# Optimization experiments

Hardware: AMD Instinct MI355X
Metric: run time of the kernel (lower is better)

The kernel has to match this reference:

```python
import jax, jax.numpy as jnp
import numpy as np
from jax.scipy.linalg import solve_triangular

B, K, N = 64, 24, 934  # batch, SMPL joints (key_size), sparse mesh points (A_size)
LAMBDA_FACTOR = 1.0


def _rodrigues(rvec):
    # rvec: [..., 3] axis-angle -> [..., 3, 3] rotation matrix (SMPL rodrigues)
    theta = jnp.maximum(jnp.linalg.norm(rvec, axis=-1, keepdims=True), 1e-8)
    a = rvec / theta
    c = jnp.cos(theta)[..., None]
    s = jnp.sin(theta)[..., None]
    ax, ay, az = a[..., 0], a[..., 1], a[..., 2]
    zero = jnp.zeros_like(ax)
    skew = jnp.stack([
        jnp.stack([zero, -az, ay], -1),
        jnp.stack([az, zero, -ax], -1),
        jnp.stack([-ay, ax, zero], -1)], -2)
    aaT = a[..., :, None] * a[..., None, :]
    eye = jnp.eye(3, dtype=rvec.dtype)
    return c * eye + s * skew + (1.0 - c) * aaT


def setup_inputs() -> dict:
    key = jax.random.key(0)
    ks = jax.random.split(key, 8)
    return {
        "uv_curr": jax.random.uniform(ks[0], (B, N, 2), jnp.float32),
        "xm_": jax.random.normal(ks[1], (B, K, N, 3), jnp.float32),
        "b_s_": jax.random.normal(ks[2], (B, K, N, 3, 10), jnp.float32) * 0.1,
        "blend_curr": jax.random.uniform(ks[3], (N, K), jnp.float32),
        "W": jax.random.uniform(ks[4], (B, N), jnp.float32) * 0.95 + 0.05,
        "m00": jnp.ones((B,), jnp.float32),
        "m11": jnp.ones((B,), jnp.float32),
        "m02": jax.random.uniform(ks[5], (B,), jnp.float32),
        "m12": jax.random.uniform(ks[6], (B,), jnp.float32),
        "pred_beta": jax.random.normal(ks[7], (B, 10), jnp.float32),
        "valid_R_list_stack": jnp.broadcast_to(jnp.eye(4, dtype=jnp.float32), (B, K, 4, 4)),
    }


def reference(uv_curr, xm_, b_s_, blend_curr, W, m00, m11, m02, m12, pred_beta, valid_R_list_stack):
    Bn, Kn, Nn = xm_.shape[0], xm_.shape[1], xm_.shape[2]
    lam = jnp.exp(jnp.log(jnp.float32(1.0 / 3.0)) * jnp.float32(LAMBDA_FACTOR))  # k0*exp(log(k0/3)*lf)

    bT = blend_curr.T[None]                      # [1,K,N]
    f0 = m00[:, None, None]                       # [B,1,1]
    f1 = m11[:, None, None]
    dxu = (m02[:, None] - uv_curr[..., 0])[:, None]  # [B,1,N]
    dyv = (m12[:, None] - uv_curr[..., 1])[:, None]

    x1 = dxu * xm_[..., 1]
    x2 = f0 * xm_[..., 2] - dxu * xm_[..., 0]
    x3 = -f0 * xm_[..., 1]
    x8 = jnp.broadcast_to(bT * f0, (Bn, Kn, Nn))
    x9 = jnp.zeros((Bn, Kn, Nn), xm_.dtype)
    x10 = jnp.broadcast_to(bT * dxu, (Bn, Kn, Nn))
    y1 = -f1 * xm_[..., 2] + dyv * xm_[..., 1]
    y2 = -dyv * xm_[..., 0]
    y3 = f1 * xm_[..., 0]
    y8 = x9
    y9 = jnp.broadcast_to(bT * f1, (Bn, Kn, Nn))
    y10 = jnp.broadcast_to(bT * dyv, (Bn, Kn, Nn))

    # shape-beta blocks: [B,K,N,10]
    x4a = f0[..., None] * b_s_[:, :, :, 0] + dxu[..., None] * b_s_[:, :, :, 2]
    y4a = f1[..., None] * b_s_[:, :, :, 1] + dyv[..., None] * b_s_[:, :, :, 2]

    b1 = -f0 * xm_[..., 0] - dxu * xm_[..., 2]
    b2 = -f1 * xm_[..., 1] - dyv * xm_[..., 2]

    # [B,K,N,6] -> [B,N,K*6]
    A1 = jnp.stack([x1, x2, x3, x8, x9, x10], -1).transpose(0, 2, 1, 3).reshape(Bn, Nn, Kn * 6)
    A2 = jnp.stack([y1, y2, y3, y8, y9, y10], -1).transpose(0, 2, 1, 3).reshape(Bn, Nn, Kn * 6)
    Wn = W[..., None]
    A_top = jnp.concatenate([Wn * A1, Wn * A2], 1)            # [B,2N,6K]
    A_sh = jnp.concatenate([Wn * x4a.sum(1), Wn * y4a.sum(1)], 1)  # [B,2N,10]
    b_top = jnp.concatenate([W * b1.sum(1), W * b2.sum(1)], 1)     # [B,2N]

    rows = 2 * Nn + 10 + 3 * Kn + 3
    cols = 6 * Kn + 10
    A = jnp.zeros((Bn, rows, cols), jnp.float32)
    A = A.at[:, :2 * Nn, :6 * Kn].set(A_top)
    A = A.at[:, :2 * Nn, 6 * Kn:].set(A_sh)
    ridx = jnp.arange(10)
    A = A.at[:, rows - 10 + ridx, cols - 10 + ridx].set(lam)  # beta regularizer
    Bv = jnp.zeros((Bn, rows), jnp.float32)
    Bv = Bv.at[:, :2 * Nn].set(b_top)
    Bv = Bv.at[:, rows - 10:].set(lam * pred_beta)

    # least squares via reduced QR (same as torch train path / lstsq solution)
    q, r = jnp.linalg.qr(A)                       # q:[B,rows,cols], r:[B,cols,cols]
    rhs = jnp.einsum('bmn,bm->bn', q, Bv)
    sol = solve_triangular(r, rhs[..., None], lower=False)[..., 0]  # [B,6K+10]

    rt6 = sol[:, :6 * Kn].reshape(Bn, Kn, 6)
    r_pred = _rodrigues(rt6[..., :3])             # [B,K,3,3]
    t_pred = rt6[..., 3:]                         # [B,K,3]
    bottom = jnp.broadcast_to(jnp.array([0.0, 0.0, 0.0, 1.0], jnp.float32), (Bn, Kn, 1, 4))
    rt_pred = jnp.concatenate([
        jnp.concatenate([r_pred, jnp.zeros((Bn, Kn, 3, 1), jnp.float32)], -1),
        bottom], -2)                               # [B,K,4,4]
    r_curr = rt_pred @ valid_R_list_stack
    beta = sol[:, -10:]
    return (r_curr, t_pred, beta, r_pred)
```

## Files before the change

kernel.cpp:

```cpp
#include <hip/hip_runtime.h>
#include <hip/hip_bf16.h>

#define Bn 64
#define Kn 24
#define Nn 934
#define NBLK 4
#define GCH 234
#define NPTS 16
#define RNDS 15
#define GPK 12090
#define PB 11
#define NPAN 14
#define ST 512
#define STR 168
#define GT 512
#define MAXT 9

#define G_BYTES ((size_t)Bn * GPK * 8)

typedef __attribute__((ext_vector_type(4))) double f64x4;

__device__ __forceinline__ int rb(int i) { return (i * (i + 1)) >> 1; }

__global__ __launch_bounds__(1024) void k_pre(
    const float* __restrict__ uv, const float* __restrict__ xm,
    const float* __restrict__ bs, const float* __restrict__ Wp,
    const float* __restrict__ m00, const float* __restrict__ m11,
    const float* __restrict__ m02, const float* __restrict__ m12,
    float* __restrict__ pre)
{
    __shared__ float smL[32][30];
    __shared__ float xsL[32][3];
    const int tid = threadIdx.x;
    const int b = blockIdx.y;
    const int n0 = blockIdx.x * 32;
    const float f0 = m00[b], f1 = m11[b], cx = m02[b], cy = m12[b];

    if (tid < 960) {
        const int ni = tid / 30, c = tid - ni * 30;
        const int nc = min(n0 + ni, Nn - 1);
        float acc = 0.0f;
        const float* bp = bs + ((size_t)(b * Kn) * Nn + nc) * 30 + c;
        #pragma unroll
        for (int k = 0; k < Kn; ++k) acc += bp[(size_t)k * Nn * 30];
        smL[ni][c] = acc;
    } else {
        const int v = tid - 960;
        #pragma unroll
        for (int rep = 0; rep < 2; ++rep) {
            const int w = v + rep * 64;
            if (w < 96) {
                const int ni = w / 3, c = w - ni * 3;
                const int nc = min(n0 + ni, Nn - 1);
                float acc = 0.0f;
                const float* xp = xm + ((size_t)(b * Kn) * Nn + nc) * 3 + c;
                #pragma unroll
                for (int k = 0; k < Kn; ++k) acc += xp[(size_t)k * Nn * 3];
                xsL[ni][c] = acc;
            }
        }
    }
    __syncthreads();

    if (tid < 704) {
        const int ni = tid / 22, e = tid - ni * 22;
        const int n = n0 + ni;
        if (n < Nn) {
            const float u = uv[((size_t)b * Nn + n) * 2 + 0];
            const float v = uv[((size_t)b * Nn + n) * 2 + 1];
            const float w = Wp[(size_t)b * Nn + n];
            const float dxu = cx - u, dyv = cy - v;
            float val;
            if (e < 10)       val = w * (f0 * smL[ni][e] + dxu * smL[ni][20 + e]);
            else if (e < 20)  val = w * (f1 * smL[ni][e] + dyv * smL[ni][e + 10]);
            else if (e == 20) val = w * (-f0 * xsL[ni][0] - dxu * xsL[ni][2]);
            else              val = w * (-f1 * xsL[ni][1] - dyv * xsL[ni][2]);
            pre[((size_t)b * Nn + n) * 22 + e] = val;
        }
    }
}

__global__ __launch_bounds__(GT, 1) void k_gram(
    const float* __restrict__ uv, const float* __restrict__ xm,
    const float* __restrict__ blend, const float* __restrict__ Wp,
    const float* __restrict__ m00, const float* __restrict__ m11,
    const float* __restrict__ m02, const float* __restrict__ m12,
    const float* __restrict__ pre, double* __restrict__ Gpk)
{
    __shared__ float rowsF[2][2 * NPTS][STR];
    const int tid = threadIdx.x;
    const int b = blockIdx.y;
    const int n0 = blockIdx.x * GCH;
    const int nEnd = min(n0 + GCH, Nn);
    const float f0 = m00[b], f1 = m11[b], cx = m02[b], cy = m12[b];

    const int pt = (tid >> 4) & 15, s = tid & 15;
    const int wave = tid >> 6, lane = tid & 63;

    const f64x4 zz = {0.0, 0.0, 0.0, 0.0};
    const f64x4 pr = __builtin_amdgcn_mfma_f64_16x16x4f64((double)lane, 1.0, zz, 0, 0, 0);
    const f64x4 pc = __builtin_amdgcn_mfma_f64_16x16x4f64(1.0, (double)lane, zz, 0, 0, 0);
    const int v0 = (int)pr[0];
    const bool ac0 = (v0 >= 96) && (v0 <= 156) && (((v0 - 96) & 3) == 0);
    const int arow = ac0 ? (lane & 15) : (lane >> 2);
    const int ak   = ac0 ? (lane >> 4) : (lane & 3);
    const int w0 = (int)pc[0];
    const bool bc0 = (w0 >= 96) && (w0 <= 156) && (((w0 - 96) & 3) == 0);
    const int bcol = bc0 ? (lane & 15) : (lane >> 2);
    const int bk   = bc0 ? (lane >> 4) : (lane & 3);
    int orow[4], ocol[4];
    #pragma unroll
    for (int r2 = 0; r2 < 4; ++r2) {
        const int vr = (int)pr[r2];
        orow[r2] = ac0 ? ((vr - 96) >> 2) : ((vr - 6) >> 4);
        const int wr = (int)pc[r2];
        ocol[r2] = bc0 ? ((wr - 96) >> 2) : ((wr - 6) >> 4);
    }

    const int t0 = (wave < 4) ? wave * 5 : 20 + (wave - 4) * 9;
    const int cnt = (wave < 4) ? 5 : 9;
    int Ia[MAXT], Ja[MAXT];
    {
        int Iv = 0, Jv = t0;
        while (Jv > Iv) { Jv -= (Iv + 1); ++Iv; }
        #pragma unroll
        for (int t = 0; t < MAXT; ++t) {
            Ia[t] = Iv; Ja[t] = Jv;
            ++Jv;
            if (Jv > Iv) { Jv = 0; ++Iv; }
        }
    }

    f64x4 acc[MAXT];
    #pragma unroll
    for (int t = 0; t < MAXT; ++t) acc[t] = (f64x4){0.0, 0.0, 0.0, 0.0};

    float pf[11];
    const bool isBd = tid < 256;

    auto PF = [&](int rnd) {
        if (!isBd) return;
        const int nc = min(n0 + rnd * NPTS + pt, Nn - 1);
        if (s < 12) {
            const int k0 = 2 * s;
            const float* xa = xm + ((size_t)(b * Kn + k0) * Nn + nc) * 3;
            const float* xb = xm + ((size_t)(b * Kn + k0 + 1) * Nn + nc) * 3;
            pf[0] = xa[0]; pf[1] = xa[1]; pf[2] = xa[2];
            pf[3] = xb[0]; pf[4] = xb[1]; pf[5] = xb[2];
            pf[6] = blend[nc * Kn + k0];
            pf[7] = blend[nc * Kn + k0 + 1];
            pf[8] = uv[((size_t)b * Nn + nc) * 2 + 0];
            pf[9] = uv[((size_t)b * Nn + nc) * 2 + 1];
            pf[10] = Wp[(size_t)b * Nn + nc];
        } else if (s < 15) {
            const int e0 = (s - 12) * 8;
            const float* pp = pre + ((size_t)b * Nn + nc) * 22;
            #pragma unroll
            for (int j = 0; j < 8; ++j) pf[j] = (e0 + j < 22) ? pp[e0 + j] : 0.0f;
        }
    };
    auto WR = [&](int rnd, int bufi) {
        if (!isBd) return;
        const int n = n0 + rnd * NPTS + pt;
        float* rx = &rowsF[bufi][2 * pt][0];
        float* ry = &rowsF[bufi][2 * pt + 1][0];
        if (s < 12) {
            #pragma unroll
            for (int jj = 0; jj < 2; ++jj) {
                float vx[6], vy[6];
                if (n < nEnd) {
                    const float x0 = pf[jj * 3 + 0], x1 = pf[jj * 3 + 1], x2 = pf[jj * 3 + 2];
                    const float dxu = cx - pf[8], dyv = cy - pf[9], w = pf[10];
                    const float wbl = w * pf[6 + jj];
                    vx[0] = w * dxu * x1; vx[1] = w * (f0 * x2 - dxu * x0); vx[2] = -w * f0 * x1;
                    vx[3] = wbl * f0;     vx[4] = 0.0f;                     vx[5] = wbl * dxu;
                    vy[0] = w * (dyv * x1 - f1 * x2); vy[1] = -w * dyv * x0; vy[2] = w * f1 * x0;
                    vy[3] = 0.0f;         vy[4] = wbl * f1;                 vy[5] = wbl * dyv;
                } else {
                    #pragma unroll
                    for (int e = 0; e < 6; ++e) { vx[e] = 0.0f; vy[e] = 0.0f; }
                }
                const int cb = 6 * (2 * s + jj);
                #pragma unroll
                for (int e = 0; e < 6; ++e) {
                    rx[cb + e] = vx[e];
                    ry[cb + e] = vy[e];
                }
            }
        } else if (s < 15) {
            const int e0 = (s - 12) * 8;
            #pragma unroll
            for (int j = 0; j < 8; ++j) {
                const int e = e0 + j;
                if (e < 22) {
                    const float val = (n < nEnd) ? pf[j] : 0.0f;
                    if (e < 10)       rx[144 + e] = val;
                    else if (e < 20)  ry[144 + (e - 10)] = val;
                    else if (e == 20) rx[154] = val;
                    else              ry[154] = val;
                }
            }
        }
    };

    for (int idx = tid; idx < 320; idx += GT) {
        const int bufi = idx / 160, rem = idx % 160;
        rowsF[bufi][rem / 5][155 + rem % 5] = 0.0f;
    }

    PF(0);
    WR(0, 0);
    PF(1);
    __syncthreads();

    for (int r = 0; r < RNDS; ++r) {
        const int cur = r & 1;
        if (r < RNDS - 1) {
            WR(r + 1, cur ^ 1);
            if (r + 2 < RNDS) PF(r + 2);
        }
        #pragma unroll
        for (int ksl = 0; ksl < 8; ++ksl) {
            const float* rowA = &rowsF[cur][4 * ksl + ak][0];
            const float* rowB = &rowsF[cur][4 * ksl + bk][0];
            #pragma unroll
            for (int t = 0; t < MAXT; ++t) {
                if (t < cnt && t0 + t < 55) {
                    const double av = (double)rowA[16 * Ia[t] + arow];
                    const double bv = (double)rowB[16 * Ja[t] + bcol];
                    acc[t] = __builtin_amdgcn_mfma_f64_16x16x4f64(av, bv, acc[t], 0, 0, 0);
                }
            }
        }
        __syncthreads();
    }

    double* Gb = Gpk + (size_t)b * GPK;
    #pragma unroll
    for (int t = 0; t < MAXT; ++t) {
        if (t < cnt && t0 + t < 55) {
            #pragma unroll
            for (int rr = 0; rr < 4; ++rr) {
                const int gi = 16 * Ia[t] + orow[rr];
                const int gj = 16 * Ja[t] + ocol[rr];
                if (gi < 155 && gj < 155 && gj <= gi)
                    unsafeAtomicAdd(&Gb[rb(gi) + gj], acc[t][rr]);
            }
        }
    }
}

__global__ __launch_bounds__(ST, 2) void k_solve(
    const float* __restrict__ pbeta, const float* __restrict__ vR,
    const double* __restrict__ Gpk, float* __restrict__ out)
{
    __shared__ double tri[12090];
    __shared__ double fd[NPAN][66];
    __shared__ double Pp[144][PB];
    __shared__ double Qq[144][PB];
    __shared__ double cv[160];
    __shared__ double xv[160];
    __shared__ double dinv[160];
    const int tid = threadIdx.x;
    const int b = blockIdx.x;
    const double lam2 = 1.0 / 9.0;
    const double* Gb = Gpk + (size_t)b * GPK;

    for (int idx = tid; idx < GPK; idx += ST) tri[idx] = Gb[idx];
    __syncthreads();
    if (tid < 10) {
        const int d = 144 + tid;
        tri[rb(d) + d] += lam2;
        tri[rb(154) + 144 + tid] += lam2 * (double)pbeta[b * 10 + tid];
    }
    __syncthreads();

    for (int p = 0; p < NPAN; ++p) {
        const int c0 = p * PB, r0 = c0 + PB;
        const int m2 = 155 - r0;

        double dblk[66], dl[PB];
        #pragma unroll
        for (int r = 0; r < PB; ++r) {
            const int baser = rb(c0 + r) + c0;
            #pragma unroll
            for (int c = 0; c <= r; ++c) dblk[r * (r + 1) / 2 + c] = tri[baser + c];
        }
        #pragma unroll
        for (int j = 0; j < PB; ++j) {
            const double invd = 1.0 / dblk[j * (j + 1) / 2 + j];
            dl[j] = invd;
            #pragma unroll
            for (int r = j + 1; r < PB; ++r) {
                const double mr = dblk[r * (r + 1) / 2 + j] * invd;
                #pragma unroll
                for (int c = j + 1; c <= r; ++c)
                    dblk[r * (r + 1) / 2 + c] -= mr * dblk[c * (c + 1) / 2 + j];
            }
        }
        if (tid == 0) {
            #pragma unroll
            for (int e = 0; e < 66; ++e) fd[p][e] = dblk[e];
            #pragma unroll
            for (int j = 0; j < PB; ++j) dinv[c0 + j] = dl[j];
        }

        for (int i = r0 + tid; i < 155; i += ST) {
            const int ip = i - r0;
            const int base = rb(i) + c0;
            double a[PB], bbv[PB];
            #pragma unroll
            for (int k = 0; k < PB; ++k) a[k] = tri[base + k];
            #pragma unroll
            for (int t = 0; t < PB; ++t) {
                const double bt = a[t] * dl[t];
                bbv[t] = bt;
                #pragma unroll
                for (int k = t + 1; k < PB; ++k)
                    a[k] -= bt * dblk[k * (k + 1) / 2 + t];
            }
            #pragma unroll
            for (int k = 0; k < PB; ++k) {
                tri[base + k] = a[k]; Pp[ip][k] = bbv[k]; Qq[ip][k] = a[k];
            }
        }
        __syncthreads();

        {
            const int th2 = (m2 + 1) >> 1;
            const int ttot = (th2 * (th2 + 1)) >> 1;
            for (int e = tid; e < ttot; e += ST) {
                int tr = (int)((sqrtf(8.0f * (float)e + 1.0f) - 1.0f) * 0.5f);
                while ((tr + 1) * (tr + 2) / 2 <= e) ++tr;
                while (tr * (tr + 1) / 2 > e) --tr;
                const int tc = e - ((tr * (tr + 1)) >> 1);
                const int rg0 = 2 * tr, cg0 = 2 * tc;
                const bool r1ok = (rg0 + 1) < m2;
                const bool c1ok = (cg0 + 1) < m2;
                double pa0[PB], pa1[PB], qb0[PB], qb1[PB];
                #pragma unroll
                for (int k = 0; k < PB; ++k) {
                    pa0[k] = Pp[rg0][k];
                    pa1[k] = r1ok ? Pp[rg0 + 1][k] : 0.0;
                    qb0[k] = Qq[cg0][k];
                    qb1[k] = c1ok ? Qq[cg0 + 1][k] : 0.0;
                }
                double s00 = 0.0, s01 = 0.0, s10 = 0.0, s11 = 0.0;
                #pragma unroll
                for (int k = 0; k < PB; ++k) {
                    s00 += pa0[k] * qb0[k];
                    s01 += pa0[k] * qb1[k];
                    s10 += pa1[k] * qb0[k];
                    s11 += pa1[k] * qb1[k];
                }
                tri[rb(r0 + rg0) + r0 + cg0] -= s00;
                if (c1ok && (cg0 + 1) <= rg0)
                    tri[rb(r0 + rg0) + r0 + cg0 + 1] -= s01;
                if (r1ok)
                    tri[rb(r0 + rg0 + 1) + r0 + cg0] -= s10;
                if (r1ok && c1ok)
                    tri[rb(r0 + rg0 + 1) + r0 + cg0 + 1] -= s11;
            }
        }
        __syncthreads();
    }

    for (int j = tid; j < 154; j += ST) xv[j] = tri[rb(154) + j] * dinv[j];
    __syncthreads();

    for (int p = NPAN - 1; p >= 0; --p) {
        const int c0 = p * PB;
        double x[PB], dl[PB];
        #pragma unroll
        for (int r = 0; r < PB; ++r) { dl[r] = dinv[c0 + r]; x[r] = xv[c0 + r]; }
        #pragma unroll
        for (int j = PB - 1; j >= 1; --j) {
            #pragma unroll
            for (int i2 = 0; i2 < j; ++i2)
                x[i2] -= dl[i2] * fd[p][j * (j + 1) / 2 + i2] * x[j];
        }
        if (tid == 0) {
            #pragma unroll
            for (int r = 0; r < PB; ++r) cv[c0 + r] = x[r];
        }
        for (int i = tid; i < c0; i += ST) {
            double sum = 0.0;
            #pragma unroll
            for (int jj = 0; jj < PB; ++jj) sum += tri[rb(c0 + jj) + i] * x[jj];
            xv[i] -= dinv[i] * sum;
        }
        __syncthreads();
    }

    if (tid < Kn) {
        const int k = tid;
        const double rxv = cv[6 * k + 0], ryv = cv[6 * k + 1], rzv = cv[6 * k + 2];
        const double t0 = cv[6 * k + 3], t1 = cv[6 * k + 4], t2 = cv[6 * k + 5];
        const double nrm = sqrt(rxv * rxv + ryv * ryv + rzv * rzv);
        const double th = fmax(nrm, 1e-8);
        const double ax = rxv / th, ay = ryv / th, az = rzv / th;
        const double c = cos(th), sn = sin(th), mc = 1.0 - c;
        double R[3][3];
        R[0][0] = c + mc * ax * ax;        R[0][1] = -sn * az + mc * ax * ay; R[0][2] =  sn * ay + mc * ax * az;
        R[1][0] =  sn * az + mc * ay * ax; R[1][1] = c + mc * ay * ay;        R[1][2] = -sn * ax + mc * ay * az;
        R[2][0] = -sn * ay + mc * az * ax; R[2][1] =  sn * ax + mc * az * ay; R[2][2] = c + mc * az * az;

        const float* VRp = vR + ((size_t)(b * Kn + k)) * 16;
        float* oc = out + ((size_t)(b * Kn + k)) * 16;
        #pragma unroll
        for (int r = 0; r < 3; ++r)
            #pragma unroll
            for (int cc = 0; cc < 4; ++cc) {
                const double val = R[r][0] * (double)VRp[0 * 4 + cc]
                                 + R[r][1] * (double)VRp[1 * 4 + cc]
                                 + R[r][2] * (double)VRp[2 * 4 + cc];
                oc[r * 4 + cc] = (float)val;
            }
        #pragma unroll
        for (int cc = 0; cc < 4; ++cc) oc[12 + cc] = VRp[12 + cc];

        float* ot = out + 24576 + ((size_t)(b * Kn + k)) * 3;
        ot[0] = (float)t0; ot[1] = (float)t1; ot[2] = (float)t2;

        float* orp = out + 29824 + ((size_t)(b * Kn + k)) * 9;
        #pragma unroll
        for (int r = 0; r < 3; ++r)
            #pragma unroll
            for (int cc = 0; cc < 3; ++cc)
                orp[r * 3 + cc] = (float)R[r][cc];
    }
    if (tid >= 32 && tid < 42) {
        out[29184 + b * 10 + (tid - 32)] = (float)cv[144 + (tid - 32)];
    }
}

extern "C" void kernel_launch(void* const* d_in, const int* in_sizes, int n_in,
                              void* d_out, int out_size, void* d_ws, size_t ws_size,
                              hipStream_t stream) {
    const float* uv    = (const float*)d_in[0];
    const float* xm    = (const float*)d_in[1];
    const float* bs    = (const float*)d_in[2];
    const float* blend = (const float*)d_in[3];
    const float* Wp    = (const float*)d_in[4];
    const float* m00   = (const float*)d_in[5];
    const float* m11   = (const float*)d_in[6];
    const float* m02   = (const float*)d_in[7];
    const float* m12   = (const float*)d_in[8];
    const float* pbeta = (const float*)d_in[9];
    const float* vRp   = (const float*)d_in[10];
    float* out = (float*)d_out;
    double* Gpk = (double*)d_ws;
    float* pre = (float*)((char*)d_ws + G_BYTES);

    hipMemsetAsync(d_ws, 0, G_BYTES, stream);

    dim3 gP((Nn + 31) / 32, Bn);
    k_pre<<<gP, 1024, 0, stream>>>(uv, xm, bs, Wp, m00, m11, m02, m12, pre);

    dim3 gG(NBLK, Bn);
    k_gram<<<gG, GT, 0, stream>>>(uv, xm, blend, Wp, m00, m11, m02, m12, pre, Gpk);

    k_solve<<<Bn, ST, 0, stream>>>(pbeta, vRp, Gpk, out);
}
```

Baseline: 229.2 us.

## Transpose Gram shared tile to column-major for vectorized MFMA operand loads

The shared-memory staging buffer for the Gram-matrix rows is transposed so that each column holds the 32 row samples contiguously (padded stride 36). Each lane can then fetch its eight k-values with two float4 LDS reads instead of eight scalar reads, and the MFMA chain per tile runs back-to-back. Each lane now sums its k-values in a different order, but the result is still the same A^T A product. The write side now scatters scalars across columns, which may cause bank conflicts there.

```diff
diff --git a/kernel.cpp b/kernel.cpp
--- a/kernel.cpp
+++ b/kernel.cpp
@@ -12,7 +12,7 @@
 #define PB 11
 #define NPAN 14
 #define ST 512
-#define STR 168
+#define CSTR 36
 #define GT 512
 #define MAXT 9
 
@@ -87,7 +87,7 @@
     const float* __restrict__ m02, const float* __restrict__ m12,
     const float* __restrict__ pre, double* __restrict__ Gpk)
 {
-    __shared__ float rowsF[2][2 * NPTS][STR];
+    __shared__ float rowsT[2][160][CSTR];
     const int tid = threadIdx.x;
     const int b = blockIdx.y;
     const int n0 = blockIdx.x * GCH;
@@ -162,8 +162,7 @@
     auto WR = [&](int rnd, int bufi) {
         if (!isBd) return;
         const int n = n0 + rnd * NPTS + pt;
-        float* rx = &rowsF[bufi][2 * pt][0];
-        float* ry = &rowsF[bufi][2 * pt + 1][0];
+        const int rx = 2 * pt, ry = 2 * pt + 1;
         if (s < 12) {
             #pragma unroll
             for (int jj = 0; jj < 2; ++jj) {
@@ -183,8 +182,8 @@
                 const int cb = 6 * (2 * s + jj);
                 #pragma unroll
                 for (int e = 0; e < 6; ++e) {
-                    rx[cb + e] = vx[e];
-                    ry[cb + e] = vy[e];
+                    rowsT[bufi][cb + e][rx] = vx[e];
+                    rowsT[bufi][cb + e][ry] = vy[e];
                 }
             }
         } else if (s < 15) {
@@ -194,10 +193,10 @@
                 const int e = e0 + j;
                 if (e < 22) {
                     const float val = (n < nEnd) ? pf[j] : 0.0f;
-                    if (e < 10)       rx[144 + e] = val;
-                    else if (e < 20)  ry[144 + (e - 10)] = val;
-                    else if (e == 20) rx[154] = val;
-                    else              ry[154] = val;
+                    if (e < 10)       rowsT[bufi][144 + e][rx] = val;
+                    else if (e < 20)  rowsT[bufi][144 + (e - 10)][ry] = val;
+                    else if (e == 20) rowsT[bufi][154][rx] = val;
+                    else              rowsT[bufi][154][ry] = val;
                 }
             }
         }
@@ -205,7 +204,7 @@
 
     for (int idx = tid; idx < 320; idx += GT) {
         const int bufi = idx / 160, rem = idx % 160;
-        rowsF[bufi][rem / 5][155 + rem % 5] = 0.0f;
+        rowsT[bufi][155 + rem / 32][rem % 32] = 0.0f;
     }
 
     PF(0);
@@ -220,16 +219,22 @@
             if (r + 2 < RNDS) PF(r + 2);
         }
         #pragma unroll
-        for (int ksl = 0; ksl < 8; ++ksl) {
-            const float* rowA = &rowsF[cur][4 * ksl + ak][0];
-            const float* rowB = &rowsF[cur][4 * ksl + bk][0];
-            #pragma unroll
-            for (int t = 0; t < MAXT; ++t) {
-                if (t < cnt && t0 + t < 55) {
-                    const double av = (double)rowA[16 * Ia[t] + arow];
-                    const double bv = (double)rowB[16 * Ja[t] + bcol];
-                    acc[t] = __builtin_amdgcn_mfma_f64_16x16x4f64(av, bv, acc[t], 0, 0, 0);
-                }
+        for (int t = 0; t < MAXT; ++t) {
+            if (t < cnt && t0 + t < 55) {
+                const float* colA = &rowsT[cur][16 * Ia[t] + arow][0];
+                const float* colB = &rowsT[cur][16 * Ja[t] + bcol][0];
+                const float4 a0 = *(const float4*)&colA[8 * ak];
+                const float4 a1 = *(const float4*)&colA[8 * ak + 4];
+                const float4 b0 = *(const float4*)&colB[8 * bk];
+                const float4 b1 = *(const float4*)&colB[8 * bk + 4];
+                acc[t] = __builtin_amdgcn_mfma_f64_16x16x4f64((double)a0.x, (double)b0.x, acc[t], 0, 0, 0);
+                acc[t] = __builtin_amdgcn_mfma_f64_16x16x4f64((double)a0.y, (double)b0.y, acc[t], 0, 0, 0);
+                acc[t] = __builtin_amdgcn_mfma_f64_16x16x4f64((double)a0.z, (double)b0.z, acc[t], 0, 0, 0);
+                acc[t] = __builtin_amdgcn_mfma_f64_16x16x4f64((double)a0.w, (double)b0.w, acc[t], 0, 0, 0);
+                acc[t] = __builtin_amdgcn_mfma_f64_16x16x4f64((double)a1.x, (double)b1.x, acc[t], 0, 0, 0);
+                acc[t] = __builtin_amdgcn_mfma_f64_16x16x4f64((double)a1.y, (double)b1.y, acc[t], 0, 0, 0);
+                acc[t] = __builtin_amdgcn_mfma_f64_16x16x4f64((double)a1.z, (double)b1.z, acc[t], 0, 0, 0);
+                acc[t] = __builtin_amdgcn_mfma_f64_16x16x4f64((double)a1.w, (double)b1.w, acc[t], 0, 0, 0);
             }
         }
         __syncthreads();
```

Result: no change. 228.0 us (-0.5%).
